# Kernel optimization log

Hardware: AMD Instinct MI355X
Metric: run time of the kernel (lower is better)

Reference implementation:

```python
import jax, jax.numpy as jnp
import numpy as np
from jax import lax

B, CIN, H, W = 32, 128, 64, 64
COUT, K, NK, HID = 128, 3, 4, 32
TEMP = 34.0
PAD = 1


def setup_inputs() -> dict:
    key = jax.random.key(0)
    k1, k2, k3, k4 = jax.random.split(key, 4)
    x = jax.random.normal(k1, (B, CIN, H, W), dtype=jnp.float32)
    fc1_w = jax.random.normal(k2, (HID, CIN), dtype=jnp.float32) * (2.0 / CIN) ** 0.5
    fc2_w = jax.random.normal(k3, (NK, HID), dtype=jnp.float32) * (2.0 / HID) ** 0.5
    fc2_b = jnp.zeros((NK,), dtype=jnp.float32)
    weight = jax.random.normal(k4, (NK, COUT, CIN, K, K), dtype=jnp.float32) * 0.05
    bias = jnp.zeros((NK, COUT), dtype=jnp.float32)
    return {"x": x, "fc1_w": fc1_w, "fc2_w": fc2_w, "fc2_b": fc2_b,
            "weight": weight, "bias": bias}


def _per_sample_conv(xi, wi):
    # xi: [CIN, H, W], wi: [COUT, CIN, K, K]
    out = lax.conv_general_dilated(
        xi[None], wi,
        window_strides=(1, 1),
        padding=[(PAD, PAD), (PAD, PAD)],
        dimension_numbers=("NCHW", "OIHW", "NCHW"))
    return out[0]  # [COUT, H', W']


def reference(x, fc1_w, fc2_w, fc2_b, weight, bias):
    # attention: global avg pool -> 1x1 conv (matmul) -> relu -> 1x1 conv -> softmax
    context = jnp.mean(x, axis=(2, 3))                      # [B, CIN]
    hid = jax.nn.relu(context @ fc1_w.T)                    # [B, HID]
    logits = hid @ fc2_w.T + fc2_b                          # [B, NK]
    att = jax.nn.softmax(logits / TEMP, axis=1)             # [B, NK]
    # aggregate per-sample kernels and biases
    agg_w = jnp.einsum("bk,koihw->boihw", att, weight)      # [B, COUT, CIN, K, K]
    agg_b = att @ bias                                      # [B, COUT]
    # per-sample convolution (equivalent to the groups=B trick in torch)
    out = jax.vmap(_per_sample_conv)(x, agg_w)              # [B, COUT, H, W]
    return out + agg_b[:, :, None, None]
```

## Files before the change

kernel.cpp:

```cpp
#include <hip/hip_runtime.h>
#include <hip/hip_bf16.h>

#define B_    32
#define CIN_  128
#define H_    64
#define W_    64
#define COUT_ 128
#define NK_   4
#define HID_  32
#define TEMP_ 34.0f

typedef short bf16x8 __attribute__((ext_vector_type(8)));
typedef short short4v __attribute__((ext_vector_type(4)));
typedef float f32x4  __attribute__((ext_vector_type(4)));
typedef float f32x16 __attribute__((ext_vector_type(16)));

__device__ __forceinline__ short f2bf(float f) {
    union { float f; unsigned u; } c; c.f = f;
    unsigned r = (c.u + 0x7FFFu + ((c.u >> 16) & 1u)) >> 16;
    return (short)r;
}
__device__ __forceinline__ float bf2f(short s) {
    union { unsigned u; float f; } c; c.u = ((unsigned)(unsigned short)s) << 16;
    return c.f;
}

#define TPAD 140
__global__ __launch_bounds__(256) void k_prep(const float* __restrict__ x,
                                              float* __restrict__ ctx,
                                              short* __restrict__ xb) {
    __shared__ short T[64 * TPAD];
    const int tid = threadIdx.x;
    const int b = blockIdx.x >> 6;
    const int h = blockIdx.x & 63;
#pragma unroll
    for (int k = 0; k < 8; ++k) {
        const int idx = k * 256 + tid;
        const int wq = idx & 15;
        const int ci = idx >> 4;
        float4 v = *(const float4*)(x + (((size_t)b * CIN_ + ci) * H_ + h) * W_ + wq * 4);
        short* p = &T[(wq * 4) * TPAD + ci];
        p[0 * TPAD] = f2bf(v.x);
        p[1 * TPAD] = f2bf(v.y);
        p[2 * TPAD] = f2bf(v.z);
        p[3 * TPAD] = f2bf(v.w);
    }
    __syncthreads();
    {
        const int ci = tid >> 1;
        const int ph = tid & 1;
        float s = 0.f;
        for (int ww = ph * 32; ww < ph * 32 + 32; ++ww) s += bf2f(T[ww * TPAD + ci]);
        s += __shfl_down(s, 1, 64);
        if (ph == 0) atomicAdd(&ctx[b * CIN_ + ci], s);
    }
    const int ww = tid >> 2;
    const int cc = tid & 3;
    short* op = xb + (((size_t)b * H_ + h) * W_ + ww) * CIN_ + cc * 32;
    const short* tp = &T[ww * TPAD + cc * 32];
#pragma unroll
    for (int k = 0; k < 4; ++k)
        *(bf16x8*)(op + k * 8) = *(const bf16x8*)(tp + k * 8);
}

__global__ void k_context(const float* __restrict__ x, float* __restrict__ ctx) {
    const int bc = blockIdx.x;
    const float* p = x + (size_t)bc * (H_ * W_);
    const int lane = threadIdx.x;
    float s = 0.f;
    for (int i = lane * 4; i < H_ * W_; i += 64 * 4) {
        float4 v = *(const float4*)(p + i);
        s += v.x + v.y + v.z + v.w;
    }
    for (int off = 32; off > 0; off >>= 1) s += __shfl_down(s, off, 64);
    if (lane == 0) ctx[bc] = s * (1.0f / (H_ * W_));
}

#define SF1S 129
__global__ __launch_bounds__(1024) void k_att(const float* __restrict__ ctx,
                      const float* __restrict__ fc1w,
                      const float* __restrict__ fc2w,
                      const float* __restrict__ fc2b,
                      const float* __restrict__ bias,
                      float* __restrict__ att, float* __restrict__ aggb,
                      float ctx_scale) {
    __shared__ float sctx[B_ * CIN_];
    __shared__ float sf1[HID_ * SF1S];
    __shared__ float shid[B_ * HID_];
    __shared__ float satt[B_ * NK_];
    const int t = threadIdx.x;
    for (int i = t; i < B_ * CIN_; i += 1024) sctx[i] = ctx[i] * ctx_scale;
    for (int i = t; i < HID_ * CIN_; i += 1024) sf1[(i >> 7) * SF1S + (i & 127)] = fc1w[i];
    __syncthreads();
    {
        const int b = t >> 5, hh = t & 31;
        float s = 0.f;
        for (int ci = 0; ci < CIN_; ++ci) s += sctx[b * CIN_ + ci] * sf1[hh * SF1S + ci];
        shid[b * HID_ + hh] = fmaxf(s, 0.f);
    }
    __syncthreads();
    if (t < B_) {
        float lg[NK_]; float mx = -1e30f;
#pragma unroll
        for (int k = 0; k < NK_; ++k) {
            float s = fc2b[k];
            for (int hh = 0; hh < HID_; ++hh) s += shid[t * HID_ + hh] * fc2w[k * HID_ + hh];
            lg[k] = s / TEMP_; mx = fmaxf(mx, lg[k]);
        }
        float den = 0.f;
#pragma unroll
        for (int k = 0; k < NK_; ++k) { lg[k] = expf(lg[k] - mx); den += lg[k]; }
        const float rd = 1.0f / den;
#pragma unroll
        for (int k = 0; k < NK_; ++k) { satt[t * NK_ + k] = lg[k] * rd; att[t * NK_ + k] = lg[k] * rd; }
    }
    __syncthreads();
    {
        const int b = t >> 5, c0 = (t & 31) * 4;
        float4 bw[NK_];
#pragma unroll
        for (int k = 0; k < NK_; ++k) bw[k] = *(const float4*)(bias + k * COUT_ + c0);
        float4 r = make_float4(0.f, 0.f, 0.f, 0.f);
#pragma unroll
        for (int k = 0; k < NK_; ++k) {
            const float a = satt[b * NK_ + k];
            r.x += a * bw[k].x; r.y += a * bw[k].y; r.z += a * bw[k].z; r.w += a * bw[k].w;
        }
        *(float4*)(aggb + b * COUT_ + c0) = r;
    }
}

__global__ void k_aggw(const float* __restrict__ att,
                       const float* __restrict__ weight,
                       short* __restrict__ aggwt) {
    const int idx = blockIdx.x * 256 + threadIdx.x;
    const int ci = idx & 127;
    const int co = (idx >> 7) & 127;
    const int b  = idx >> 14;
    const float a0 = att[b * NK_ + 0];
    const float a1 = att[b * NK_ + 1];
    const float a2 = att[b * NK_ + 2];
    const float a3 = att[b * NK_ + 3];
    const float* w0 = weight + ((size_t)co * CIN_ + ci) * 9;
    const float* w1 = w0 + (size_t)COUT_ * CIN_ * 9;
    const float* w2 = w1 + (size_t)COUT_ * CIN_ * 9;
    const float* w3 = w2 + (size_t)COUT_ * CIN_ * 9;
    short* o = aggwt + ((size_t)(b * COUT_ + co) * 9) * CIN_ + ci;
#pragma unroll
    for (int r = 0; r < 9; ++r)
        o[r * CIN_] = f2bf(a0 * w0[r] + a1 * w1[r] + a2 * w2[r] + a3 * w3[r]);
}

#define RBY 8448
#define RSH 4224
__global__ __launch_bounds__(256, 2) void k_conv(const short* __restrict__ xb,
        const short* __restrict__ aggwt, const float* __restrict__ aggb,
        float* __restrict__ out) {
    __shared__ short xt[6 * RSH];
    const int tid = threadIdx.x;
    const int blk = blockIdx.x;
    const int b = blk & 31;
    const int h0 = (blk >> 5) * 4;
    const int lane = tid & 63;
    const int wv = tid >> 6;
    const int l31 = lane & 31;
    const int lane5 = lane >> 5;

    if (tid < 96) {
        const int row = tid >> 4;
        const int q = tid & 15;
        const int cl = (q < 8) ? q : (512 + q);
        *(int4*)(&xt[row * RSH + cl * 8]) = make_int4(0, 0, 0, 0);
    }

    f32x16 acc[8];
#pragma unroll
    for (int t = 0; t < 8; ++t)
#pragma unroll
        for (int k = 0; k < 16; ++k) acc[t][k] = 0.f;

    const short* Ap = aggwt + (size_t)(b * COUT_ + wv * 32 + l31) * 9 * CIN_ + lane5 * 8;

    for (int half = 0; half < 2; ++half) {
#pragma unroll
        for (int k = 0; k < 12; ++k) {
            const int cbase = k * 256 + wv * 64;
            const int row = cbase >> 9;
            const int clb = (cbase & 511) + 8;
            const int in_h = h0 - 1 + row;
            short* dst = &xt[row * RSH + clb * 8];
            if (in_h >= 0 && in_h < H_) {
                const int cl = clb + lane;
                const int s = cl >> 3;
                const int p = cl & 7;
                const int wp = s - 1;
                const int ci8 = half * 8 + ((p - wp) & 7);
                const short* gp = xb + (((size_t)b * H_ + in_h) * W_ + wp) * CIN_ + ci8 * 8;
                __builtin_amdgcn_global_load_lds(
                    (const __attribute__((address_space(1))) void*)gp,
                    (__attribute__((address_space(3))) void*)dst, 16, 0, 0);
            } else {
                *(int4*)(dst + lane * 8) = make_int4(0, 0, 0, 0);
            }
        }
        __syncthreads();

#pragma unroll
        for (int kcl = 0; kcl < 4; ++kcl) {
            const int kc = half * 4 + kcl;
            bf16x8 av[9];
#pragma unroll
            for (int r = 0; r < 9; ++r)
                av[r] = *(const bf16x8*)(Ap + kc * 16 + r * CIN_);
#pragma unroll
            for (int ir = 0; ir < 6; ++ir) {
                bf16x8 bv[2][3];
#pragma unroll
                for (int i = 0; i < 2; ++i)
#pragma unroll
                    for (int kw = 0; kw < 3; ++kw) {
                        const int s = i * 32 + l31 + kw;
                        const int off = 16 * ((2 * kcl + lane5 + s - 1) & 7);
                        bv[i][kw] = *(const bf16x8*)((const char*)xt + ir * RBY + s * 128 + off);
                    }
#pragma unroll
                for (int orr = 0; orr < 4; ++orr) {
                    if (orr <= ir && ir <= orr + 2) {
                        const int kh = ir - orr;
#pragma unroll
                        for (int i = 0; i < 2; ++i)
#pragma unroll
                            for (int kw = 0; kw < 3; ++kw)
                                acc[orr * 2 + i] = __builtin_amdgcn_mfma_f32_32x32x16_bf16(
                                    av[kh * 3 + kw], bv[i][kw], acc[orr * 2 + i], 0, 0, 0);
                    }
                }
            }
        }
        if (half == 0) __syncthreads();
    }

    const float* ab = aggb + b * COUT_;
#pragma unroll
    for (int orr = 0; orr < 4; ++orr) {
#pragma unroll
        for (int i = 0; i < 2; ++i) {
            const int hh = h0 + orr;
            const int w = i * 32 + l31;
            float* op = out + ((size_t)b * COUT_ * H_ + hh) * W_ + w;
            const f32x16 a = acc[orr * 2 + i];
#pragma unroll
            for (int reg = 0; reg < 16; ++reg) {
                const int co = wv * 32 + (reg & 3) + 8 * (reg >> 2) + 4 * lane5;
                op[(size_t)co * (H_ * W_)] = a[reg] + ab[co];
            }
        }
    }
}

#define LDS_S 136
__global__ __launch_bounds__(256) void k_conv_fb(const float* __restrict__ x,
                                              const short* __restrict__ aggwt,
                                              const float* __restrict__ aggb,
                                              float* __restrict__ out) {
    __shared__ short xs[3 * 66 * LDS_S];
    const int tid = threadIdx.x;
    const int b = blockIdx.x >> 6;
    const int h = blockIdx.x & 63;
    for (int i = tid; i < 3 * 32 * 16; i += 256) {
        const int hr  = i >> 9;
        const int rem = i & 511;
        const int ci4 = rem >> 4;
        const int wb  = rem & 15;
        const int ih = h + hr - 1;
        float4 v0 = make_float4(0.f, 0.f, 0.f, 0.f), v1 = v0, v2 = v0, v3 = v0;
        if (ih >= 0 && ih < H_) {
            const float* base = x + (((size_t)b * CIN_ + ci4 * 4) * H_ + ih) * W_ + wb * 4;
            v0 = *(const float4*)(base);
            v1 = *(const float4*)(base + H_ * W_);
            v2 = *(const float4*)(base + 2 * H_ * W_);
            v3 = *(const float4*)(base + 3 * H_ * W_);
        }
        short* p = &xs[(hr * 66 + 1 + wb * 4) * LDS_S + ci4 * 4];
        short4v s0 = { f2bf(v0.x), f2bf(v1.x), f2bf(v2.x), f2bf(v3.x) };
        short4v s1 = { f2bf(v0.y), f2bf(v1.y), f2bf(v2.y), f2bf(v3.y) };
        short4v s2 = { f2bf(v0.z), f2bf(v1.z), f2bf(v2.z), f2bf(v3.z) };
        short4v s3 = { f2bf(v0.w), f2bf(v1.w), f2bf(v2.w), f2bf(v3.w) };
        *(short4v*)(p + 0 * LDS_S) = s0;
        *(short4v*)(p + 1 * LDS_S) = s1;
        *(short4v*)(p + 2 * LDS_S) = s2;
        *(short4v*)(p + 3 * LDS_S) = s3;
        short4v z = { 0, 0, 0, 0 };
        if (wb == 0)  *(short4v*)(&xs[(hr * 66 + 0) * LDS_S + ci4 * 4]) = z;
        if (wb == 15) *(short4v*)(&xs[(hr * 66 + 65) * LDS_S + ci4 * 4]) = z;
    }
    __syncthreads();
    const int lane = tid & 63;
    const int wave = tid >> 6;
    const int quad = lane >> 4;
    const int l16  = lane & 15;
    f32x4 acc[2][4];
#pragma unroll
    for (int i = 0; i < 2; ++i)
#pragma unroll
        for (int j = 0; j < 4; ++j) acc[i][j] = (f32x4){0.f, 0.f, 0.f, 0.f};
    const short* A0 = aggwt + (size_t)(b * COUT_ + wave * 32 + l16) * 9 * CIN_;
    const short* A1 = A0 + 16 * 9 * CIN_;
    for (int r = 0; r < 9; ++r) {
        const int kh = r / 3, kw = r % 3;
#pragma unroll
        for (int c = 0; c < 4; ++c) {
            const int k0 = c * 32 + quad * 8;
            bf16x8 a0 = *(const bf16x8*)(A0 + r * CIN_ + k0);
            bf16x8 a1 = *(const bf16x8*)(A1 + r * CIN_ + k0);
#pragma unroll
            for (int nt = 0; nt < 4; ++nt) {
                const int col = nt * 16 + l16 + kw;
                bf16x8 bv = *(const bf16x8*)(&xs[(kh * 66 + col) * LDS_S + k0]);
                acc[0][nt] = __builtin_amdgcn_mfma_f32_16x16x32_bf16(a0, bv, acc[0][nt], 0, 0, 0);
                acc[1][nt] = __builtin_amdgcn_mfma_f32_16x16x32_bf16(a1, bv, acc[1][nt], 0, 0, 0);
            }
        }
    }
    float* outb = out + (size_t)b * COUT_ * H_ * W_ + h * W_;
    const float* ab = aggb + b * COUT_;
#pragma unroll
    for (int mt = 0; mt < 2; ++mt)
#pragma unroll
        for (int rr = 0; rr < 4; ++rr) {
            const int co = wave * 32 + mt * 16 + quad * 4 + rr;
            const float bb = ab[co];
#pragma unroll
            for (int nt = 0; nt < 4; ++nt)
                outb[(size_t)co * (H_ * W_) + nt * 16 + l16] = acc[mt][nt][rr] + bb;
        }
}

extern "C" void kernel_launch(void* const* d_in, const int* in_sizes, int n_in,
                              void* d_out, int out_size, void* d_ws, size_t ws_size,
                              hipStream_t stream) {
    const float* x    = (const float*)d_in[0];
    const float* fc1w = (const float*)d_in[1];
    const float* fc2w = (const float*)d_in[2];
    const float* fc2b = (const float*)d_in[3];
    const float* wgt  = (const float*)d_in[4];
    const float* bias = (const float*)d_in[5];
    float* out = (float*)d_out;

    char* ws = (char*)d_ws;
    float* ctx   = (float*)(ws + 0);
    float* att   = (float*)(ws + 16384);
    float* aggb  = (float*)(ws + 16896);
    short* aggwt = (short*)(ws + 65536);
    short* xb    = (short*)(ws + 9502720);
    const size_t NEED = 9502720u + 33554432u;

    if (ws_size >= NEED) {
        hipMemsetAsync(ctx, 0, B_ * CIN_ * sizeof(float), stream);
        k_prep<<<dim3(B_ * H_), dim3(256), 0, stream>>>(x, ctx, xb);
        k_att<<<dim3(1), dim3(1024), 0, stream>>>(ctx, fc1w, fc2w, fc2b, bias, att, aggb,
                                                  1.0f / (H_ * W_));
        k_aggw<<<dim3((B_ * COUT_ * CIN_) / 256), dim3(256), 0, stream>>>(att, wgt, aggwt);
        k_conv<<<dim3(B_ * (H_ / 4)), dim3(256), 0, stream>>>(xb, aggwt, aggb, out);
    } else {
        k_context<<<dim3(B_ * CIN_), dim3(64), 0, stream>>>(x, ctx);
        k_att<<<dim3(1), dim3(1024), 0, stream>>>(ctx, fc1w, fc2w, fc2b, bias, att, aggb, 1.0f);
        k_aggw<<<dim3((B_ * COUT_ * CIN_) / 256), dim3(256), 0, stream>>>(att, wgt, aggwt);
        k_conv_fb<<<dim3(B_ * H_), dim3(256), 0, stream>>>(x, aggwt, aggb, out);
    }
}
```

Baseline: 190.6 us.

## Drop bf16 NHWC prepass; convert fp32 input inside conv and fuse attention into aggw

Removes the k_prep pass that wrote a bf16 channels-last copy of x, the memset, and the single-block k_att kernel. The conv kernel now reads fp32 NCHW input directly, converts it to bf16 and writes it into the swizzled LDS layout. Each aggw block recomputes the attention MLP and softmax for its own sample. This saves a full read and write of the input plus two launches, at the cost of strided, non-async fp32 loads inside the conv and redundant attention work in every aggw block.

```diff
diff --git a/kernel.cpp b/kernel.cpp
--- a/kernel.cpp
+++ b/kernel.cpp
@@ -1,5 +1,4 @@
 #include <hip/hip_runtime.h>
-#include <hip/hip_bf16.h>
 
 #define B_    32
 #define CIN_  128
@@ -11,8 +10,6 @@
 #define TEMP_ 34.0f
 
 typedef short bf16x8 __attribute__((ext_vector_type(8)));
-typedef short short4v __attribute__((ext_vector_type(4)));
-typedef float f32x4  __attribute__((ext_vector_type(4)));
 typedef float f32x16 __attribute__((ext_vector_type(16)));
 
 __device__ __forceinline__ short f2bf(float f) {
@@ -20,50 +17,9 @@
     unsigned r = (c.u + 0x7FFFu + ((c.u >> 16) & 1u)) >> 16;
     return (short)r;
 }
-__device__ __forceinline__ float bf2f(short s) {
-    union { unsigned u; float f; } c; c.u = ((unsigned)(unsigned short)s) << 16;
-    return c.f;
-}
-
-#define TPAD 140
-__global__ __launch_bounds__(256) void k_prep(const float* __restrict__ x,
-                                              float* __restrict__ ctx,
-                                              short* __restrict__ xb) {
-    __shared__ short T[64 * TPAD];
-    const int tid = threadIdx.x;
-    const int b = blockIdx.x >> 6;
-    const int h = blockIdx.x & 63;
-#pragma unroll
-    for (int k = 0; k < 8; ++k) {
-        const int idx = k * 256 + tid;
-        const int wq = idx & 15;
-        const int ci = idx >> 4;
-        float4 v = *(const float4*)(x + (((size_t)b * CIN_ + ci) * H_ + h) * W_ + wq * 4);
-        short* p = &T[(wq * 4) * TPAD + ci];
-        p[0 * TPAD] = f2bf(v.x);
-        p[1 * TPAD] = f2bf(v.y);
-        p[2 * TPAD] = f2bf(v.z);
-        p[3 * TPAD] = f2bf(v.w);
-    }
-    __syncthreads();
-    {
-        const int ci = tid >> 1;
-        const int ph = tid & 1;
-        float s = 0.f;
-        for (int ww = ph * 32; ww < ph * 32 + 32; ++ww) s += bf2f(T[ww * TPAD + ci]);
-        s += __shfl_down(s, 1, 64);
-        if (ph == 0) atomicAdd(&ctx[b * CIN_ + ci], s);
-    }
-    const int ww = tid >> 2;
-    const int cc = tid & 3;
-    short* op = xb + (((size_t)b * H_ + h) * W_ + ww) * CIN_ + cc * 32;
-    const short* tp = &T[ww * TPAD + cc * 32];
-#pragma unroll
-    for (int k = 0; k < 4; ++k)
-        *(bf16x8*)(op + k * 8) = *(const bf16x8*)(tp + k * 8);
-}
-
-__global__ void k_context(const float* __restrict__ x, float* __restrict__ ctx) {
+
+__global__ __launch_bounds__(64) void k_context(const float* __restrict__ x,
+                                                float* __restrict__ ctx) {
     const int bc = blockIdx.x;
     const float* p = x + (size_t)bc * (H_ * W_);
     const int lane = threadIdx.x;
@@ -76,35 +32,40 @@
     if (lane == 0) ctx[bc] = s * (1.0f / (H_ * W_));
 }
 
-#define SF1S 129
-__global__ __launch_bounds__(1024) void k_att(const float* __restrict__ ctx,
-                      const float* __restrict__ fc1w,
-                      const float* __restrict__ fc2w,
-                      const float* __restrict__ fc2b,
-                      const float* __restrict__ bias,
-                      float* __restrict__ att, float* __restrict__ aggb,
-                      float ctx_scale) {
-    __shared__ float sctx[B_ * CIN_];
-    __shared__ float sf1[HID_ * SF1S];
-    __shared__ float shid[B_ * HID_];
-    __shared__ float satt[B_ * NK_];
-    const int t = threadIdx.x;
-    for (int i = t; i < B_ * CIN_; i += 1024) sctx[i] = ctx[i] * ctx_scale;
-    for (int i = t; i < HID_ * CIN_; i += 1024) sf1[(i >> 7) * SF1S + (i & 127)] = fc1w[i];
+__global__ __launch_bounds__(256) void k_aggw(const float* __restrict__ ctx,
+        const float* __restrict__ fc1w, const float* __restrict__ fc2w,
+        const float* __restrict__ fc2b, const float* __restrict__ bias,
+        const float* __restrict__ weight, short* __restrict__ aggwt,
+        float* __restrict__ aggb) {
+    __shared__ float hidp[8][32];
+    __shared__ float shid[32];
+    __shared__ float satt[NK_];
+    const int tid = threadIdx.x;
+    const int blk = blockIdx.x;
+    const int b = blk >> 6;
+    {
+        const int hh = tid & 31, part = tid >> 5;
+        const float* c  = ctx + b * CIN_ + part * 16;
+        const float* f1 = fc1w + hh * CIN_ + part * 16;
+        float s = 0.f;
+#pragma unroll
+        for (int j = 0; j < 16; ++j) s += c[j] * f1[j];
+        hidp[part][hh] = s;
+    }
     __syncthreads();
-    {
-        const int b = t >> 5, hh = t & 31;
+    if (tid < 32) {
         float s = 0.f;
-        for (int ci = 0; ci < CIN_; ++ci) s += sctx[b * CIN_ + ci] * sf1[hh * SF1S + ci];
-        shid[b * HID_ + hh] = fmaxf(s, 0.f);
+#pragma unroll
+        for (int p = 0; p < 8; ++p) s += hidp[p][tid];
+        shid[tid] = fmaxf(s, 0.f);
     }
     __syncthreads();
-    if (t < B_) {
+    if (tid == 0) {
         float lg[NK_]; float mx = -1e30f;
 #pragma unroll
         for (int k = 0; k < NK_; ++k) {
             float s = fc2b[k];
-            for (int hh = 0; hh < HID_; ++hh) s += shid[t * HID_ + hh] * fc2w[k * HID_ + hh];
+            for (int hh = 0; hh < HID_; ++hh) s += shid[hh] * fc2w[k * HID_ + hh];
             lg[k] = s / TEMP_; mx = fmaxf(mx, lg[k]);
         }
         float den = 0.f;
@@ -112,35 +73,18 @@
         for (int k = 0; k < NK_; ++k) { lg[k] = expf(lg[k] - mx); den += lg[k]; }
         const float rd = 1.0f / den;
 #pragma unroll
-        for (int k = 0; k < NK_; ++k) { satt[t * NK_ + k] = lg[k] * rd; att[t * NK_ + k] = lg[k] * rd; }
+        for (int k = 0; k < NK_; ++k) satt[k] = lg[k] * rd;
     }
     __syncthreads();
-    {
-        const int b = t >> 5, c0 = (t & 31) * 4;
-        float4 bw[NK_];
-#pragma unroll
-        for (int k = 0; k < NK_; ++k) bw[k] = *(const float4*)(bias + k * COUT_ + c0);
-        float4 r = make_float4(0.f, 0.f, 0.f, 0.f);
-#pragma unroll
-        for (int k = 0; k < NK_; ++k) {
-            const float a = satt[b * NK_ + k];
-            r.x += a * bw[k].x; r.y += a * bw[k].y; r.z += a * bw[k].z; r.w += a * bw[k].w;
-        }
-        *(float4*)(aggb + b * COUT_ + c0) = r;
-    }
-}
-
-__global__ void k_aggw(const float* __restrict__ att,
-                       const float* __restrict__ weight,
-                       short* __restrict__ aggwt) {
-    const int idx = blockIdx.x * 256 + threadIdx.x;
+    const float a0 = satt[0], a1 = satt[1], a2 = satt[2], a3 = satt[3];
+
+    const int idx = blk * 256 + tid;
     const int ci = idx & 127;
     const int co = (idx >> 7) & 127;
-    const int b  = idx >> 14;
-    const float a0 = att[b * NK_ + 0];
-    const float a1 = att[b * NK_ + 1];
-    const float a2 = att[b * NK_ + 2];
-    const float a3 = att[b * NK_ + 3];
+    if ((tid & 127) == 0)
+        aggb[b * COUT_ + co] = a0 * bias[co] + a1 * bias[COUT_ + co]
+                             + a2 * bias[2 * COUT_ + co] + a3 * bias[3 * COUT_ + co];
+
     const float* w0 = weight + ((size_t)co * CIN_ + ci) * 9;
     const float* w1 = w0 + (size_t)COUT_ * CIN_ * 9;
     const float* w2 = w1 + (size_t)COUT_ * CIN_ * 9;
@@ -153,7 +97,7 @@
 
 #define RBY 8448
 #define RSH 4224
-__global__ __launch_bounds__(256, 2) void k_conv(const short* __restrict__ xb,
+__global__ __launch_bounds__(256, 2) void k_conv(const float* __restrict__ x,
         const short* __restrict__ aggwt, const float* __restrict__ aggb,
         float* __restrict__ out) {
     __shared__ short xt[6 * RSH];
@@ -182,26 +126,23 @@
     const short* Ap = aggwt + (size_t)(b * COUT_ + wv * 32 + l31) * 9 * CIN_ + lane5 * 8;
 
     for (int half = 0; half < 2; ++half) {
+        const int cib = half * 64;
 #pragma unroll
         for (int k = 0; k < 12; ++k) {
-            const int cbase = k * 256 + wv * 64;
-            const int row = cbase >> 9;
-            const int clb = (cbase & 511) + 8;
+            const int task = k * 4 + wv;
+            const int row = task >> 3;
+            const int g = task & 7;
             const int in_h = h0 - 1 + row;
-            short* dst = &xt[row * RSH + clb * 8];
+            bf16x8 v = (bf16x8){0, 0, 0, 0, 0, 0, 0, 0};
             if (in_h >= 0 && in_h < H_) {
-                const int cl = clb + lane;
-                const int s = cl >> 3;
-                const int p = cl & 7;
-                const int wp = s - 1;
-                const int ci8 = half * 8 + ((p - wp) & 7);
-                const short* gp = xb + (((size_t)b * H_ + in_h) * W_ + wp) * CIN_ + ci8 * 8;
-                __builtin_amdgcn_global_load_lds(
-                    (const __attribute__((address_space(1))) void*)gp,
-                    (__attribute__((address_space(3))) void*)dst, 16, 0, 0);
-            } else {
-                *(int4*)(dst + lane * 8) = make_int4(0, 0, 0, 0);
+                const float* gp = x + (((size_t)b * CIN_ + cib + g * 8) * H_ + in_h) * W_ + lane;
+                float f[8];
+#pragma unroll
+                for (int j = 0; j < 8; ++j) f[j] = gp[j * (H_ * W_)];
+#pragma unroll
+                for (int j = 0; j < 8; ++j) v[j] = f2bf(f[j]);
             }
+            *(bf16x8*)(&xt[row * RSH + ((lane + 1) * 8 + ((g + lane) & 7)) * 8]) = v;
         }
         __syncthreads();
 
@@ -256,84 +197,6 @@
             }
         }
     }
-}
-
-#define LDS_S 136
-__global__ __launch_bounds__(256) void k_conv_fb(const float* __restrict__ x,
-                                              const short* __restrict__ aggwt,
-                                              const float* __restrict__ aggb,
-                                              float* __restrict__ out) {
-    __shared__ short xs[3 * 66 * LDS_S];
-    const int tid = threadIdx.x;
-    const int b = blockIdx.x >> 6;
-    const int h = blockIdx.x & 63;
-    for (int i = tid; i < 3 * 32 * 16; i += 256) {
-        const int hr  = i >> 9;
-        const int rem = i & 511;
-        const int ci4 = rem >> 4;
-        const int wb  = rem & 15;
-        const int ih = h + hr - 1;
-        float4 v0 = make_float4(0.f, 0.f, 0.f, 0.f), v1 = v0, v2 = v0, v3 = v0;
-        if (ih >= 0 && ih < H_) {
-            const float* base = x + (((size_t)b * CIN_ + ci4 * 4) * H_ + ih) * W_ + wb * 4;
-            v0 = *(const float4*)(base);
-            v1 = *(const float4*)(base + H_ * W_);
-            v2 = *(const float4*)(base + 2 * H_ * W_);
-            v3 = *(const float4*)(base + 3 * H_ * W_);
-        }
-        short* p = &xs[(hr * 66 + 1 + wb * 4) * LDS_S + ci4 * 4];
-        short4v s0 = { f2bf(v0.x), f2bf(v1.x), f2bf(v2.x), f2bf(v3.x) };
-        short4v s1 = { f2bf(v0.y), f2bf(v1.y), f2bf(v2.y), f2bf(v3.y) };
-        short4v s2 = { f2bf(v0.z), f2bf(v1.z), f2bf(v2.z), f2bf(v3.z) };
-        short4v s3 = { f2bf(v0.w), f2bf(v1.w), f2bf(v2.w), f2bf(v3.w) };
-        *(short4v*)(p + 0 * LDS_S) = s0;
-        *(short4v*)(p + 1 * LDS_S) = s1;
-        *(short4v*)(p + 2 * LDS_S) = s2;
-        *(short4v*)(p + 3 * LDS_S) = s3;
-        short4v z = { 0, 0, 0, 0 };
-        if (wb == 0)  *(short4v*)(&xs[(hr * 66 + 0) * LDS_S + ci4 * 4]) = z;
-        if (wb == 15) *(short4v*)(&xs[(hr * 66 + 65) * LDS_S + ci4 * 4]) = z;
-    }
-    __syncthreads();
-    const int lane = tid & 63;
-    const int wave = tid >> 6;
-    const int quad = lane >> 4;
-    const int l16  = lane & 15;
-    f32x4 acc[2][4];
-#pragma unroll
-    for (int i = 0; i < 2; ++i)
-#pragma unroll
-        for (int j = 0; j < 4; ++j) acc[i][j] = (f32x4){0.f, 0.f, 0.f, 0.f};
-    const short* A0 = aggwt + (size_t)(b * COUT_ + wave * 32 + l16) * 9 * CIN_;
-    const short* A1 = A0 + 16 * 9 * CIN_;
-    for (int r = 0; r < 9; ++r) {
-        const int kh = r / 3, kw = r % 3;
-#pragma unroll
-        for (int c = 0; c < 4; ++c) {
-            const int k0 = c * 32 + quad * 8;
-            bf16x8 a0 = *(const bf16x8*)(A0 + r * CIN_ + k0);
-            bf16x8 a1 = *(const bf16x8*)(A1 + r * CIN_ + k0);
-#pragma unroll
-            for (int nt = 0; nt < 4; ++nt) {
-                const int col = nt * 16 + l16 + kw;
-                bf16x8 bv = *(const bf16x8*)(&xs[(kh * 66 + col) * LDS_S + k0]);
-                acc[0][nt] = __builtin_amdgcn_mfma_f32_16x16x32_bf16(a0, bv, acc[0][nt], 0, 0, 0);
-                acc[1][nt] = __builtin_amdgcn_mfma_f32_16x16x32_bf16(a1, bv, acc[1][nt], 0, 0, 0);
-            }
-        }
-    }
-    float* outb = out + (size_t)b * COUT_ * H_ * W_ + h * W_;
-    const float* ab = aggb + b * COUT_;
-#pragma unroll
-    for (int mt = 0; mt < 2; ++mt)
-#pragma unroll
-        for (int rr = 0; rr < 4; ++rr) {
-            const int co = wave * 32 + mt * 16 + quad * 4 + rr;
-            const float bb = ab[co];
-#pragma unroll
-            for (int nt = 0; nt < 4; ++nt)
-                outb[(size_t)co * (H_ * W_) + nt * 16 + l16] = acc[mt][nt][rr] + bb;
-        }
 }
 
 extern "C" void kernel_launch(void* const* d_in, const int* in_sizes, int n_in,
@@ -349,23 +212,11 @@
 
     char* ws = (char*)d_ws;
     float* ctx   = (float*)(ws + 0);
-    float* att   = (float*)(ws + 16384);
-    float* aggb  = (float*)(ws + 16896);
+    float* aggb  = (float*)(ws + 16384);
     short* aggwt = (short*)(ws + 65536);
-    short* xb    = (short*)(ws + 9502720);
-    const size_t NEED = 9502720u + 33554432u;
-
-    if (ws_size >= NEED) {
-        hipMemsetAsync(ctx, 0, B_ * CIN_ * sizeof(float), stream);
-        k_prep<<<dim3(B_ * H_), dim3(256), 0, stream>>>(x, ctx, xb);
-        k_att<<<dim3(1), dim3(1024), 0, stream>>>(ctx, fc1w, fc2w, fc2b, bias, att, aggb,
-                                                  1.0f / (H_ * W_));
-        k_aggw<<<dim3((B_ * COUT_ * CIN_) / 256), dim3(256), 0, stream>>>(att, wgt, aggwt);
-        k_conv<<<dim3(B_ * (H_ / 4)), dim3(256), 0, stream>>>(xb, aggwt, aggb, out);
-    } else {
-        k_context<<<dim3(B_ * CIN_), dim3(64), 0, stream>>>(x, ctx);
-        k_att<<<dim3(1), dim3(1024), 0, stream>>>(ctx, fc1w, fc2w, fc2b, bias, att, aggb, 1.0f);
-        k_aggw<<<dim3((B_ * COUT_ * CIN_) / 256), dim3(256), 0, stream>>>(att, wgt, aggwt);
-        k_conv_fb<<<dim3(B_ * H_), dim3(256), 0, stream>>>(x, aggwt, aggb, out);
-    }
-}
+
+    k_context<<<dim3(B_ * CIN_), dim3(64), 0, stream>>>(x, ctx);
+    k_aggw<<<dim3((B_ * COUT_ * CIN_) / 256), dim3(256), 0, stream>>>(
+        ctx, fc1w, fc2w, fc2b, bias, wgt, aggwt, aggb);
+    k_conv<<<dim3(B_ * (H_ / 4)), dim3(256), 0, stream>>>(x, aggwt, aggb, out);
+}
```

Measured after the change: 171.2 us. 10.2% less time.
